# Optimization experiments

Measured on AMD Instinct MI355X. Metric: run time of the kernel, lower is better.

The kernel has to match this reference:

```python
import jax, jax.numpy as jnp
import numpy as np

RATIO = 4

def positional_encoding(d_model, max_len, w_s):
    # w_s: (B,) per-example frequency warp. pe[b, p, 0::2]=sin, pe[b, p, 1::2]=cos
    pos = jnp.arange(max_len, dtype=jnp.float32)                      # (L,)
    div = jnp.power(10000.0, jnp.arange(0, d_model, 2, dtype=jnp.float32) / d_model)  # (d/2,)
    ang = w_s[:, None, None] * pos[None, :, None] / div[None, None, :]  # (B, L, d/2)
    pe = jnp.stack([jnp.sin(ang), jnp.cos(ang)], axis=-1)             # (B, L, d/2, 2)
    return pe.reshape(w_s.shape[0], max_len, d_model)

def setup_inputs() -> dict:
    key = jax.random.key(0)
    ks = jax.random.split(key, 6)
    B, Tds, L, D = 32, 2048, 512, 256
    q = jax.random.normal(ks[0], (B, Tds, D), dtype=jnp.float32)
    k = jax.random.normal(ks[1], (B, L, D), dtype=jnp.float32)
    v = jax.random.normal(ks[2], (B, L, D), dtype=jnp.float32)
    w_compress = jax.random.normal(ks[3], (D // RATIO, D), dtype=jnp.float32) * (D ** -0.5)
    text_lengths = jax.random.randint(ks[4], (B,), L // 2, L + 1).at[0].set(L)
    mel_lengths = jax.random.randint(ks[5], (B,), (Tds * RATIO) // 2, Tds * RATIO + 1).at[0].set(Tds * RATIO)
    return {"q": q, "k": k, "v": v, "w_compress": w_compress,
            "text_lengths": text_lengths, "mel_lengths": mel_lengths}

def reference(q, k, v, w_compress, text_lengths, mel_lengths):
    B, Tds, D = q.shape
    L = k.shape[1]
    # padding masks (True = padded)
    text_mask = jnp.arange(L)[None, :] >= text_lengths[:, None]            # (B, L)
    mel_mask_ds = jnp.arange(Tds)[None, :] >= (mel_lengths // RATIO)[:, None]  # (B, Tds)
    # positional encodings
    q = q + positional_encoding(D, Tds, jnp.ones((B,), dtype=jnp.float32))
    w_s = mel_lengths.astype(jnp.float32) / RATIO / text_lengths.astype(jnp.float32)
    k = k + positional_encoding(D, L, w_s)
    q = q * (float(D) ** -0.5)
    # scores + masked softmax over text axis
    scores = jnp.einsum('btd,bld->btl', q, k)                              # (B, Tds, L)
    scores = jnp.where(text_mask[:, None, :], -jnp.inf, scores)
    align = jax.nn.softmax(scores, axis=-1)
    align = jnp.where(mel_mask_ds[:, :, None], 0.0, align)
    # hard argmax one-hot, straight-through blend
    idx = jnp.argmax(align, axis=-1)                                       # (B, Tds)
    align_oh = jax.nn.one_hot(idx, L, dtype=align.dtype)
    align_oh = jnp.where(mel_mask_ds[:, :, None], 0.0, align_oh)
    blend = align + jax.lax.stop_gradient(align_oh - align)
    attn = jnp.einsum('btl,bld->btd', blend, v)                            # (B, Tds, D)
    # Compress (Linear D -> D//ratio, no bias) then transpose(1,2)
    out = jnp.einsum('btd,cd->bct', attn, w_compress)                      # (B, D//ratio, Tds)
    return out, align
```

## Files before the change

### kernel.cpp

```cpp
#include <hip/hip_runtime.h>
#include <math.h>

#define NB  32
#define TDS 2048
#define LL  512
#define DD  256
#define DC  64
#define GAP_THR 4e-4f

typedef __attribute__((ext_vector_type(8)))  short short8;
typedef __attribute__((ext_vector_type(16))) float f32x16;
typedef __attribute__((ext_vector_type(4)))  float f32x4;

__device__ __forceinline__ unsigned short f2bf(float x) {
    union { float f; unsigned u; } v; v.f = x;
    unsigned r = v.u + 0x7fffu + ((v.u >> 16) & 1u);
    return (unsigned short)(r >> 16);
}
__device__ __forceinline__ float bf2f(unsigned short h) {
    union { unsigned u; float f; } v; v.u = ((unsigned)h) << 16;
    return v.f;
}


__global__ void peq_kernel(float* __restrict__ peq, int* __restrict__ cnt) {
    int idx = blockIdx.x * 256 + threadIdx.x;
    if (idx == 0) cnt[0] = 0;
    int t = idx >> 8;
    int d = idx & 255;
    int i = d >> 1;
    double invdiv = exp((double)i * (-9.210340371976184 / 128.0));
    double ang = (double)t * invdiv;
    double s, c;
    sincos(ang, &s, &c);
    peq[idx] = (float)((d & 1) ? c : s);
}

__global__ __launch_bounds__(256)
void pek_kernel(const float* __restrict__ k,
                const int* __restrict__ text_lengths,
                const int* __restrict__ mel_lengths,
                char* __restrict__ kps) {
    __shared__ double invdiv[128];
    const int tid = threadIdx.x;
    if (tid < 128) invdiv[tid] = exp((double)tid * (-9.210340371976184 / 128.0));
    __syncthreads();
    int f = blockIdx.x * 256 + tid;
    int b = f >> 14;
    int r = f & 16383;
    int ks = r >> 11;
    int r2 = r & 2047;
    int cs = r2 >> 7;
    int r3 = r2 & 127;
    int kh = r3 >> 6;
    int g  = (r3 >> 5) & 1;
    int lane32 = r3 & 31;
    int l  = cs * 32 + lane32;
    int k0 = ks * 32 + kh * 16 + g * 8;
    const float* kr = k + ((size_t)(b * LL + l)) * DD + k0;
    float4 kv0 = *(const float4*)(kr);
    float4 kv1 = *(const float4*)(kr + 4);
    float kv[8] = {kv0.x, kv0.y, kv0.z, kv0.w, kv1.x, kv1.y, kv1.z, kv1.w};
    double wsd = ((double)mel_lengths[b] * 0.25) / (double)text_lengths[b];
    double base_ang = wsd * (double)l;
    unsigned short h[8], lo8[8];
#pragma unroll
    for (int jj = 0; jj < 4; ++jj) {
        int i = (k0 >> 1) + jj;
        double ang = base_ang * invdiv[i];
        double n = rint(ang * 0.15915494309189535);
        double red = fma(n, -6.283185307179586, ang);
        float sn, cs2;
        sincosf((float)red, &sn, &cs2);
        float e0 = kv[2 * jj] + sn;
        float e1 = kv[2 * jj + 1] + cs2;
        h[2 * jj]       = f2bf(e0);
        h[2 * jj + 1]   = f2bf(e1);
        lo8[2 * jj]     = f2bf(e0 - bf2f(h[2 * jj]));
        lo8[2 * jj + 1] = f2bf(e1 - bf2f(h[2 * jj + 1]));
    }
    size_t off = (size_t)b * 524288 + (size_t)ks * 65536 + (size_t)cs * 4096
               + kh * 1024 + g * 512 + lane32 * 16;
    uint4 hv, lv;
    hv.x = h[0] | ((unsigned)h[1] << 16); hv.y = h[2] | ((unsigned)h[3] << 16);
    hv.z = h[4] | ((unsigned)h[5] << 16); hv.w = h[6] | ((unsigned)h[7] << 16);
    lv.x = lo8[0] | ((unsigned)lo8[1] << 16); lv.y = lo8[2] | ((unsigned)lo8[3] << 16);
    lv.z = lo8[4] | ((unsigned)lo8[5] << 16); lv.w = lo8[6] | ((unsigned)lo8[7] << 16);
    *(uint4*)(kps + off) = hv;
    *(uint4*)(kps + off + 2048) = lv;
}

__global__ __launch_bounds__(256, 4)
void score_kernel(const float* __restrict__ q,
                  const float* __restrict__ peq,
                  const char* __restrict__ kps,
                  const int* __restrict__ text_lengths,
                  const int* __restrict__ mel_lengths,
                  float* __restrict__ align_out,
                  int* __restrict__ idx_out,
                  int* __restrict__ flag_cnt,
                  int* __restrict__ flags) {
    __shared__ alignas(16) char smA[32768];
    struct Epi {
        float v1[4][32]; int i1[4][32]; float v2[4][32];
        float S[4][32];  float M[32];
    };
    __shared__ Epi ep;

    const int wgid = blockIdx.x;
    const int xcd = wgid & 7, loc = wgid >> 3;
    const int nid = xcd * 256 + loc;
    const int b  = nid >> 6;
    const int t0 = (nid & 63) << 5;

    const int tid = threadIdx.x;
    const int wn = tid >> 6, lane = tid & 63;
    const int c31 = lane & 31, hi5 = lane >> 5;
    const int tlen = text_lengths[b];
    const int melq = mel_lengths[b] >> 2;

    const char* kpb = kps + (size_t)b * 524288 + (size_t)(hi5 * 512 + c31 * 16);

    f32x16 acc[4];
#pragma unroll
    for (int ci = 0; ci < 4; ++ci)
#pragma unroll
        for (int rg = 0; rg < 16; ++rg) acc[ci][rg] = 0.f;

#define BLOAD(dst, ksv, civ)                                                    \
    {                                                                           \
        const char* p = kpb + (ksv) * 65536 + (wn * 4 + (civ)) * 4096;          \
        dst[0] = *(const short8*)(p);                                           \
        dst[1] = *(const short8*)(p + 1024);                                    \
        dst[2] = *(const short8*)(p + 2048);                                    \
        dst[3] = *(const short8*)(p + 3072);                                    \
    }
#define MFMA6(CI, B)                                                            \
    {                                                                           \
        acc[CI] = __builtin_amdgcn_mfma_f32_32x32x16_bf16(ah0, B[0], acc[CI], 0, 0, 0); \
        acc[CI] = __builtin_amdgcn_mfma_f32_32x32x16_bf16(ah0, B[2], acc[CI], 0, 0, 0); \
        acc[CI] = __builtin_amdgcn_mfma_f32_32x32x16_bf16(al0, B[0], acc[CI], 0, 0, 0); \
        acc[CI] = __builtin_amdgcn_mfma_f32_32x32x16_bf16(ah1, B[1], acc[CI], 0, 0, 0); \
        acc[CI] = __builtin_amdgcn_mfma_f32_32x32x16_bf16(ah1, B[3], acc[CI], 0, 0, 0); \
        acc[CI] = __builtin_amdgcn_mfma_f32_32x32x16_bf16(al1, B[1], acc[CI], 0, 0, 0); \
    }

    short8 B0[4], B1[4];
    BLOAD(B0, 0, 0)

    {
        const int sr = tid >> 3, kc = tid & 7;
        const float* qr = q   + ((size_t)(b * TDS) + t0 + sr) * DD;
        const float* pr = peq + (size_t)(t0 + sr) * DD;
#pragma unroll
        for (int kq = 0; kq < 4; ++kq) {
            int m = kq * 8 + kc;
            int k0 = m * 8;
            float4 qa = *(const float4*)(qr + k0);
            float4 qb4 = *(const float4*)(qr + k0 + 4);
            float4 pa = *(const float4*)(pr + k0);
            float4 pb = *(const float4*)(pr + k0 + 4);
            float e[8] = {(qa.x + pa.x) * 0.0625f, (qa.y + pa.y) * 0.0625f,
                          (qa.z + pa.z) * 0.0625f, (qa.w + pa.w) * 0.0625f,
                          (qb4.x + pb.x) * 0.0625f, (qb4.y + pb.y) * 0.0625f,
                          (qb4.z + pb.z) * 0.0625f, (qb4.w + pb.w) * 0.0625f};
            unsigned short h[8], lo[8];
#pragma unroll
            for (int j = 0; j < 8; ++j) {
                h[j] = f2bf(e[j]);
                lo[j] = f2bf(e[j] - bf2f(h[j]));
            }
            uint4 hv, lv;
            hv.x = h[0] | ((unsigned)h[1] << 16); hv.y = h[2] | ((unsigned)h[3] << 16);
            hv.z = h[4] | ((unsigned)h[5] << 16); hv.w = h[6] | ((unsigned)h[7] << 16);
            lv.x = lo[0] | ((unsigned)lo[1] << 16); lv.y = lo[2] | ((unsigned)lo[3] << 16);
            lv.z = lo[4] | ((unsigned)lo[5] << 16); lv.w = lo[6] | ((unsigned)lo[7] << 16);
            int base = (m >> 2) * 4096 + ((m >> 1) & 1) * 1024 + (m & 1) * 512 + sr * 16;
            *(uint4*)(smA + base) = hv;
            *(uint4*)(smA + base + 2048) = lv;
        }
    }
    __syncthreads();

    const int afr = hi5 * 512 + c31 * 16;
    for (int ks = 0; ks < 8; ++ks) {
        const char* ab = smA + ks * 4096 + afr;
        short8 ah0 = *(const short8*)(ab);
        short8 ah1 = *(const short8*)(ab + 1024);
        short8 al0 = *(const short8*)(ab + 2048);
        short8 al1 = *(const short8*)(ab + 3072);
        BLOAD(B1, ks, 1)
        MFMA6(0, B0)
        BLOAD(B0, ks, 2)
        MFMA6(1, B1)
        BLOAD(B1, ks, 3)
        MFMA6(2, B0)
        if (ks < 7) BLOAD(B0, ks + 1, 0)
        MFMA6(3, B1)
    }
#undef BLOAD
#undef MFMA6

    const float NEGINF = -__builtin_inff();
#pragma unroll
    for (int ci = 0; ci < 4; ++ci) {
        int col = wn * 128 + ci * 32 + c31;
        if (col >= tlen) {
#pragma unroll
            for (int rg = 0; rg < 16; ++rg) acc[ci][rg] = NEGINF;
        }
    }
    float v1[16]; int i1[16]; float v2[16];
#pragma unroll
    for (int rg = 0; rg < 16; ++rg) {
        v1[rg] = acc[0][rg]; i1[rg] = wn * 128 + c31; v2[rg] = NEGINF;
#pragma unroll
        for (int ci = 1; ci < 4; ++ci) {
            float v = acc[ci][rg]; int col = wn * 128 + ci * 32 + c31;
            if (v > v1[rg]) { v2[rg] = v1[rg]; v1[rg] = v; i1[rg] = col; }
            else if (v > v2[rg]) v2[rg] = v;
        }
    }
#pragma unroll
    for (int off = 1; off <= 16; off <<= 1) {
#pragma unroll
        for (int rg = 0; rg < 16; ++rg) {
            float ov1 = __shfl_xor(v1[rg], off, 64);
            int   oi1 = __shfl_xor(i1[rg], off, 64);
            float ov2 = __shfl_xor(v2[rg], off, 64);
            if (ov1 > v1[rg]) { v2[rg] = fmaxf(v1[rg], ov2); v1[rg] = ov1; i1[rg] = oi1; }
            else if (ov1 < v1[rg]) { v2[rg] = fmaxf(v2[rg], ov1); }
            else { i1[rg] = min(i1[rg], oi1); v2[rg] = v1[rg]; }
        }
    }
    if (c31 == 0) {
#pragma unroll
        for (int rg = 0; rg < 16; ++rg) {
            int r32 = (rg & 3) + 8 * (rg >> 2) + 4 * hi5;
            ep.v1[wn][r32] = v1[rg]; ep.i1[wn][r32] = i1[rg]; ep.v2[wn][r32] = v2[rg];
        }
    }
    __syncthreads();
    {
        const int r32 = c31;
        float V1 = ep.v1[0][r32]; int I1 = ep.i1[0][r32]; float V2 = ep.v2[0][r32];
#pragma unroll
        for (int w = 1; w < 4; ++w) {
            float cv1 = ep.v1[w][r32]; int ci1 = ep.i1[w][r32]; float cv2 = ep.v2[w][r32];
            if (cv1 > V1) { V2 = fmaxf(V1, cv2); V1 = cv1; I1 = ci1; }
            else if (cv1 < V1) { V2 = fmaxf(V2, cv1); }
            else { V2 = V1; }
        }
        if (wn == 0 && hi5 == 0) {
            int t = t0 + r32;
            idx_out[b * TDS + t] = I1;
            if (t < melq && (V1 - V2) < GAP_THR) {
                int pos = atomicAdd(flag_cnt, 1);
                flags[pos] = (b << 11) | t;
            }
            ep.M[r32] = V1;
        }
    }
    __syncthreads();
    float ssum[16];
#pragma unroll
    for (int rg = 0; rg < 16; ++rg) {
        int r32 = (rg & 3) + 8 * (rg >> 2) + 4 * hi5;
        float M = ep.M[r32];
        float s = 0.f;
#pragma unroll
        for (int ci = 0; ci < 4; ++ci) {
            float p = __expf(acc[ci][rg] - M);
            acc[ci][rg] = p; s += p;
        }
        ssum[rg] = s;
    }
#pragma unroll
    for (int off = 1; off <= 16; off <<= 1)
#pragma unroll
        for (int rg = 0; rg < 16; ++rg) ssum[rg] += __shfl_xor(ssum[rg], off, 64);
    if (c31 == 0) {
#pragma unroll
        for (int rg = 0; rg < 16; ++rg) {
            int r32 = (rg & 3) + 8 * (rg >> 2) + 4 * hi5;
            ep.S[wn][r32] = ssum[rg];
        }
    }
    __syncthreads();
#pragma unroll
    for (int rg = 0; rg < 16; ++rg) {
        int r32 = (rg & 3) + 8 * (rg >> 2) + 4 * hi5;
        int t = t0 + r32;
        float denom = ep.S[0][r32] + ep.S[1][r32] + ep.S[2][r32] + ep.S[3][r32];
        float sc = (t < melq) ? (1.0f / denom) : 0.f;
        size_t obase = ((size_t)(b * TDS + t)) * LL + wn * 128 + c31;
#pragma unroll
        for (int ci = 0; ci < 4; ++ci)
            __builtin_nontemporal_store(acc[ci][rg] * sc, align_out + obase + ci * 32);
    }
}

__global__ __launch_bounds__(256)
void refine_kernel(const float* __restrict__ q,
                   const float* __restrict__ k,
                   const int* __restrict__ text_lengths,
                   const int* __restrict__ mel_lengths,
                   const int* __restrict__ flags,
                   const int* __restrict__ flag_cnt,
                   int* __restrict__ idx_out) {
    __shared__ double qd[DD];
    __shared__ double invdiv[128];
    __shared__ double rbest[4];
    __shared__ int    ribest[4];
    const int tid = threadIdx.x;
    if (tid < 128)
        invdiv[tid] = 1.0 / pow(10000.0, (double)tid * (1.0 / 128.0));
    const int cnt = flag_cnt[0];
    for (int r = blockIdx.x; r < cnt; r += gridDim.x) {
        const int code = flags[r];
        const int b = code >> 11, t = code & 2047;
        const int tlen = text_lengths[b];
        const double ws = ((double)mel_lengths[b] * 0.25) / (double)text_lengths[b];
        __syncthreads();
        {
            const int d = tid, i = d >> 1;
            double ang = (double)t * invdiv[i];
            double sn, cs;
            sincos(ang, &sn, &cs);
            qd[d] = ((double)q[((size_t)b * TDS + t) * DD + d] + ((d & 1) ? cs : sn)) * 0.0625;
        }
        __syncthreads();
        double best = -1.0e300; int bi = 0x7fffffff;
        for (int p = 0; p < 2; ++p) {
            const int l = tid + p * 256;
            if (l < tlen) {
                const float* kr = k + ((size_t)b * LL + l) * DD;
                const double wl = ws * (double)l;
                double sacc = 0.0;
                for (int i = 0; i < 128; ++i) {
                    double ang = wl * invdiv[i];
                    double sn, cs;
                    sincos(ang, &sn, &cs);
                    sacc += ((double)kr[2 * i]     + sn) * qd[2 * i];
                    sacc += ((double)kr[2 * i + 1] + cs) * qd[2 * i + 1];
                }
                if (sacc > best || (sacc == best && l < bi)) { best = sacc; bi = l; }
            }
        }
        for (int off = 1; off <= 32; off <<= 1) {
            double ov = __shfl_xor(best, off, 64);
            int   oi = __shfl_xor(bi, off, 64);
            if (ov > best || (ov == best && oi < bi)) { best = ov; bi = oi; }
        }
        const int wv = tid >> 6;
        if ((tid & 63) == 0) { rbest[wv] = best; ribest[wv] = bi; }
        __syncthreads();
        if (tid == 0) {
            double bb = rbest[0]; int ii = ribest[0];
            for (int w = 1; w < 4; ++w)
                if (rbest[w] > bb || (rbest[w] == bb && ribest[w] < ii)) { bb = rbest[w]; ii = ribest[w]; }
            idx_out[b * TDS + t] = ii;
        }
    }
}

__global__ __launch_bounds__(256, 4)
void compress_kernel(const float* __restrict__ v,
                     const float* __restrict__ wc,
                     const int* __restrict__ idx_in,
                     const int* __restrict__ mel_lengths,
                     float* __restrict__ out) {
    __shared__ float Ws[256 * 68];
    __shared__ float Vs[16 * 132];
    __shared__ int   idxs[128];
    const int b   = blockIdx.y;
    const int t0  = blockIdx.x * 128;
    const int tid = threadIdx.x;
    const int melq = mel_lengths[b] >> 2;
    const float* vb = v + (size_t)b * LL * DD;

    if (tid < 128) {
        int t = t0 + tid;
        int ii = idx_in[b * TDS + t];
        idxs[tid] = (t >= melq) ? -1 : ii;
    }
#pragma unroll
    for (int r = 0; r < 16; ++r) {
        int f = tid + r * 256;
        int c = f >> 6;
        int u = f & 63;
        float4 wv = *(const float4*)(wc + (size_t)c * DD + u * 4);
        Ws[(u * 4 + 0) * 68 + c] = wv.x;
        Ws[(u * 4 + 1) * 68 + c] = wv.y;
        Ws[(u * 4 + 2) * 68 + c] = wv.z;
        Ws[(u * 4 + 3) * 68 + c] = wv.w;
    }

    const int tx = tid & 7;
    const int ty = tid >> 3;
    const int tv = tid >> 2;
    const int uv = tid & 3;
    float acc[8][4];
#pragma unroll
    for (int i = 0; i < 8; ++i)
#pragma unroll
        for (int j = 0; j < 4; ++j) acc[i][j] = 0.f;

    for (int ks = 0; ks < 16; ++ks) {
        const int d0 = ks * 16;
        __syncthreads();
#pragma unroll
        for (int p = 0; p < 2; ++p) {
            int t = tv + p * 64;
            int row = idxs[t];
            float4 vv = make_float4(0.f, 0.f, 0.f, 0.f);
            if (row >= 0) vv = *(const float4*)(vb + (size_t)row * DD + d0 + uv * 4);
            Vs[(uv * 4 + 0) * 132 + t] = vv.x;
            Vs[(uv * 4 + 1) * 132 + t] = vv.y;
            Vs[(uv * 4 + 2) * 132 + t] = vv.z;
            Vs[(uv * 4 + 3) * 132 + t] = vv.w;
        }
        __syncthreads();
#pragma unroll
        for (int kk = 0; kk < 16; ++kk) {
            const float* wrow = Ws + (size_t)(d0 + kk) * 68 + tx * 8;
            float4 a0 = *(const float4*)(wrow);
            float4 a1 = *(const float4*)(wrow + 4);
            float4 bb = *(const float4*)(Vs + kk * 132 + ty * 4);
            const float av[8] = {a0.x, a0.y, a0.z, a0.w, a1.x, a1.y, a1.z, a1.w};
            const float bv[4] = {bb.x, bb.y, bb.z, bb.w};
#pragma unroll
            for (int i = 0; i < 8; ++i)
#pragma unroll
                for (int j = 0; j < 4; ++j)
                    acc[i][j] = fmaf(av[i], bv[j], acc[i][j]);
        }
    }
#pragma unroll
    for (int ci = 0; ci < 8; ++ci) {
        int c = tx * 8 + ci;
        f32x4 o = {acc[ci][0], acc[ci][1], acc[ci][2], acc[ci][3]};
        __builtin_nontemporal_store(o, (f32x4*)(out + ((size_t)(b * DC + c)) * TDS + t0 + ty * 4));
    }
}

extern "C" void kernel_launch(void* const* d_in, const int* in_sizes, int n_in,
                              void* d_out, int out_size, void* d_ws, size_t ws_size,
                              hipStream_t stream) {
    const float* q    = (const float*)d_in[0];
    const float* k    = (const float*)d_in[1];
    const float* v    = (const float*)d_in[2];
    const float* wc   = (const float*)d_in[3];
    const int*   text = (const int*)d_in[4];
    const int*   mel  = (const int*)d_in[5];

    float* out   = (float*)d_out;
    float* align = out + (size_t)NB * DC * TDS;

    char*  wsb = (char*)d_ws;
    char*  KPS = wsb;
    float* PEQ = (float*)(wsb + 16777216);
    int*   IDX = (int*)(wsb + 16777216 + 2097152);
    int*   CNT = IDX + (size_t)NB * TDS;
    int*   FLG = CNT + 1;

    hipLaunchKernelGGL(peq_kernel, dim3(TDS * DD / 256), dim3(256), 0, stream, PEQ, CNT);
    hipLaunchKernelGGL(pek_kernel, dim3(NB * 16384 / 256), dim3(256), 0, stream,
                       k, text, mel, KPS);
    hipLaunchKernelGGL(score_kernel, dim3(2048), dim3(256), 0, stream,
                       q, PEQ, KPS, text, mel, align, IDX, CNT, FLG);
    hipLaunchKernelGGL(refine_kernel, dim3(256), dim3(256), 0, stream,
                       q, k, text, mel, FLG, CNT, IDX);
    hipLaunchKernelGGL(compress_kernel, dim3(TDS / 128, NB), dim3(256), 0, stream,
                       v, wc, IDX, mel, out);
}
```

Before: 223.4 us.

## Double score tile rows per block and shrink compress tiles with streamed weights

The score kernel now uses 512-thread blocks covering 64 query rows, with two row-groups of four waves each. Each group shares the same K fragments, so K traffic from global/L2 is halved, at the cost of doubling A-tile LDS to 64KB and lowering occupancy. The compress kernel drops its full 64KB transposed weight staging in favour of streaming 16-wide weight slices per k-step, uses 64-column tiles with a 2-column-per-thread micro-tile, and replaces nontemporal float4 stores with plain float2 stores. This cuts LDS use and raises block count, but adds more global weight reloads and lowers register-level reuse.

```diff
diff --git a/kernel.cpp b/kernel.cpp
--- a/kernel.cpp
+++ b/kernel.cpp
@@ -10,7 +10,6 @@
 
 typedef __attribute__((ext_vector_type(8)))  short short8;
 typedef __attribute__((ext_vector_type(16))) float f32x16;
-typedef __attribute__((ext_vector_type(4)))  float f32x4;
 
 __device__ __forceinline__ unsigned short f2bf(float x) {
     union { float f; unsigned u; } v; v.f = x;
@@ -90,7 +89,7 @@
     *(uint4*)(kps + off + 2048) = lv;
 }
 
-__global__ __launch_bounds__(256, 4)
+__global__ __launch_bounds__(512, 2)
 void score_kernel(const float* __restrict__ q,
                   const float* __restrict__ peq,
                   const char* __restrict__ kps,
@@ -100,21 +99,22 @@
                   int* __restrict__ idx_out,
                   int* __restrict__ flag_cnt,
                   int* __restrict__ flags) {
-    __shared__ alignas(16) char smA[32768];
+    __shared__ alignas(16) char smA[65536];
     struct Epi {
-        float v1[4][32]; int i1[4][32]; float v2[4][32];
-        float S[4][32];  float M[32];
+        float v1[2][4][32]; int i1[2][4][32]; float v2[2][4][32];
+        float S[2][4][32];  float M[2][32];
     };
     __shared__ Epi ep;
 
     const int wgid = blockIdx.x;
     const int xcd = wgid & 7, loc = wgid >> 3;
-    const int nid = xcd * 256 + loc;
-    const int b  = nid >> 6;
-    const int t0 = (nid & 63) << 5;
+    const int nid = xcd * 128 + loc;
+    const int b  = nid >> 5;
+    const int t0 = (nid & 31) << 6;
 
     const int tid = threadIdx.x;
-    const int wn = tid >> 6, lane = tid & 63;
+    const int wid = tid >> 6, lane = tid & 63;
+    const int wm = wid >> 2, wn = wid & 3;
     const int c31 = lane & 31, hi5 = lane >> 5;
     const int tlen = text_lengths[b];
     const int melq = mel_lengths[b] >> 2;
@@ -175,16 +175,17 @@
             hv.z = h[4] | ((unsigned)h[5] << 16); hv.w = h[6] | ((unsigned)h[7] << 16);
             lv.x = lo[0] | ((unsigned)lo[1] << 16); lv.y = lo[2] | ((unsigned)lo[3] << 16);
             lv.z = lo[4] | ((unsigned)lo[5] << 16); lv.w = lo[6] | ((unsigned)lo[7] << 16);
-            int base = (m >> 2) * 4096 + ((m >> 1) & 1) * 1024 + (m & 1) * 512 + sr * 16;
+            int base = (m >> 2) * 8192 + (sr >> 5) * 4096 + ((m >> 1) & 1) * 1024
+                     + (m & 1) * 512 + (sr & 31) * 16;
             *(uint4*)(smA + base) = hv;
             *(uint4*)(smA + base + 2048) = lv;
         }
     }
     __syncthreads();
 
-    const int afr = hi5 * 512 + c31 * 16;
+    const int afr = wm * 4096 + hi5 * 512 + c31 * 16;
     for (int ks = 0; ks < 8; ++ks) {
-        const char* ab = smA + ks * 4096 + afr;
+        const char* ab = smA + ks * 8192 + afr;
         short8 ah0 = *(const short8*)(ab);
         short8 ah1 = *(const short8*)(ab + 1024);
         short8 al0 = *(const short8*)(ab + 2048);
@@ -237,28 +238,28 @@
 #pragma unroll
         for (int rg = 0; rg < 16; ++rg) {
             int r32 = (rg & 3) + 8 * (rg >> 2) + 4 * hi5;
-            ep.v1[wn][r32] = v1[rg]; ep.i1[wn][r32] = i1[rg]; ep.v2[wn][r32] = v2[rg];
+            ep.v1[wm][wn][r32] = v1[rg]; ep.i1[wm][wn][r32] = i1[rg]; ep.v2[wm][wn][r32] = v2[rg];
         }
     }
     __syncthreads();
     {
         const int r32 = c31;
-        float V1 = ep.v1[0][r32]; int I1 = ep.i1[0][r32]; float V2 = ep.v2[0][r32];
+        float V1 = ep.v1[wm][0][r32]; int I1 = ep.i1[wm][0][r32]; float V2 = ep.v2[wm][0][r32];
 #pragma unroll
         for (int w = 1; w < 4; ++w) {
-            float cv1 = ep.v1[w][r32]; int ci1 = ep.i1[w][r32]; float cv2 = ep.v2[w][r32];
+            float cv1 = ep.v1[wm][w][r32]; int ci1 = ep.i1[wm][w][r32]; float cv2 = ep.v2[wm][w][r32];
             if (cv1 > V1) { V2 = fmaxf(V1, cv2); V1 = cv1; I1 = ci1; }
             else if (cv1 < V1) { V2 = fmaxf(V2, cv1); }
             else { V2 = V1; }
         }
         if (wn == 0 && hi5 == 0) {
-            int t = t0 + r32;
+            int t = t0 + wm * 32 + r32;
             idx_out[b * TDS + t] = I1;
             if (t < melq && (V1 - V2) < GAP_THR) {
                 int pos = atomicAdd(flag_cnt, 1);
                 flags[pos] = (b << 11) | t;
             }
-            ep.M[r32] = V1;
+            ep.M[wm][r32] = V1;
         }
     }
     __syncthreads();
@@ -266,7 +267,7 @@
 #pragma unroll
     for (int rg = 0; rg < 16; ++rg) {
         int r32 = (rg & 3) + 8 * (rg >> 2) + 4 * hi5;
-        float M = ep.M[r32];
+        float M = ep.M[wm][r32];
         float s = 0.f;
 #pragma unroll
         for (int ci = 0; ci < 4; ++ci) {
@@ -283,15 +284,15 @@
 #pragma unroll
         for (int rg = 0; rg < 16; ++rg) {
             int r32 = (rg & 3) + 8 * (rg >> 2) + 4 * hi5;
-            ep.S[wn][r32] = ssum[rg];
+            ep.S[wm][wn][r32] = ssum[rg];
         }
     }
     __syncthreads();
 #pragma unroll
     for (int rg = 0; rg < 16; ++rg) {
         int r32 = (rg & 3) + 8 * (rg >> 2) + 4 * hi5;
-        int t = t0 + r32;
-        float denom = ep.S[0][r32] + ep.S[1][r32] + ep.S[2][r32] + ep.S[3][r32];
+        int t = t0 + wm * 32 + r32;
+        float denom = ep.S[wm][0][r32] + ep.S[wm][1][r32] + ep.S[wm][2][r32] + ep.S[wm][3][r32];
         float sc = (t < melq) ? (1.0f / denom) : 0.f;
         size_t obase = ((size_t)(b * TDS + t)) * LL + wn * 128 + c31;
 #pragma unroll
@@ -364,83 +365,72 @@
     }
 }
 
-__global__ __launch_bounds__(256, 4)
+__global__ __launch_bounds__(256)
 void compress_kernel(const float* __restrict__ v,
                      const float* __restrict__ wc,
                      const int* __restrict__ idx_in,
                      const int* __restrict__ mel_lengths,
                      float* __restrict__ out) {
-    __shared__ float Ws[256 * 68];
-    __shared__ float Vs[16 * 132];
-    __shared__ int   idxs[128];
+    __shared__ float Ws[16 * 68];
+    __shared__ float Vs[16 * 68];
+    __shared__ int   idxs[64];
     const int b   = blockIdx.y;
-    const int t0  = blockIdx.x * 128;
+    const int t0  = blockIdx.x * 64;
     const int tid = threadIdx.x;
     const int melq = mel_lengths[b] >> 2;
     const float* vb = v + (size_t)b * LL * DD;
 
-    if (tid < 128) {
+    if (tid < 64) {
         int t = t0 + tid;
         int ii = idx_in[b * TDS + t];
         idxs[tid] = (t >= melq) ? -1 : ii;
     }
-#pragma unroll
-    for (int r = 0; r < 16; ++r) {
-        int f = tid + r * 256;
-        int c = f >> 6;
-        int u = f & 63;
-        float4 wv = *(const float4*)(wc + (size_t)c * DD + u * 4);
-        Ws[(u * 4 + 0) * 68 + c] = wv.x;
-        Ws[(u * 4 + 1) * 68 + c] = wv.y;
-        Ws[(u * 4 + 2) * 68 + c] = wv.z;
-        Ws[(u * 4 + 3) * 68 + c] = wv.w;
-    }
-
-    const int tx = tid & 7;
-    const int ty = tid >> 3;
-    const int tv = tid >> 2;
-    const int uv = tid & 3;
-    float acc[8][4];
-#pragma unroll
-    for (int i = 0; i < 8; ++i)
-#pragma unroll
-        for (int j = 0; j < 4; ++j) acc[i][j] = 0.f;
+
+    const int tx = tid >> 5;
+    const int ty = tid & 31;
+    const int sc = tid >> 2;
+    const int su = tid & 3;
+    float acc[8][2];
+#pragma unroll
+    for (int i = 0; i < 8; ++i) { acc[i][0] = 0.f; acc[i][1] = 0.f; }
 
     for (int ks = 0; ks < 16; ++ks) {
         const int d0 = ks * 16;
         __syncthreads();
-#pragma unroll
-        for (int p = 0; p < 2; ++p) {
-            int t = tv + p * 64;
-            int row = idxs[t];
+        {
+            float4 wv = *(const float4*)(wc + (size_t)sc * DD + d0 + su * 4);
+            Ws[(su * 4 + 0) * 68 + sc] = wv.x;
+            Ws[(su * 4 + 1) * 68 + sc] = wv.y;
+            Ws[(su * 4 + 2) * 68 + sc] = wv.z;
+            Ws[(su * 4 + 3) * 68 + sc] = wv.w;
+            int row = idxs[sc];
             float4 vv = make_float4(0.f, 0.f, 0.f, 0.f);
-            if (row >= 0) vv = *(const float4*)(vb + (size_t)row * DD + d0 + uv * 4);
-            Vs[(uv * 4 + 0) * 132 + t] = vv.x;
-            Vs[(uv * 4 + 1) * 132 + t] = vv.y;
-            Vs[(uv * 4 + 2) * 132 + t] = vv.z;
-            Vs[(uv * 4 + 3) * 132 + t] = vv.w;
+            if (row >= 0) vv = *(const float4*)(vb + (size_t)row * DD + d0 + su * 4);
+            Vs[(su * 4 + 0) * 68 + sc] = vv.x;
+            Vs[(su * 4 + 1) * 68 + sc] = vv.y;
+            Vs[(su * 4 + 2) * 68 + sc] = vv.z;
+            Vs[(su * 4 + 3) * 68 + sc] = vv.w;
         }
         __syncthreads();
 #pragma unroll
         for (int kk = 0; kk < 16; ++kk) {
-            const float* wrow = Ws + (size_t)(d0 + kk) * 68 + tx * 8;
+            const float* wrow = Ws + kk * 68 + tx * 8;
             float4 a0 = *(const float4*)(wrow);
             float4 a1 = *(const float4*)(wrow + 4);
-            float4 bb = *(const float4*)(Vs + kk * 132 + ty * 4);
+            float2 bb = *(const float2*)(Vs + kk * 68 + ty * 2);
             const float av[8] = {a0.x, a0.y, a0.z, a0.w, a1.x, a1.y, a1.z, a1.w};
-            const float bv[4] = {bb.x, bb.y, bb.z, bb.w};
-#pragma unroll
-            for (int i = 0; i < 8; ++i)
-#pragma unroll
-                for (int j = 0; j < 4; ++j)
-                    acc[i][j] = fmaf(av[i], bv[j], acc[i][j]);
-        }
-    }
-#pragma unroll
-    for (int ci = 0; ci < 8; ++ci) {
-        int c = tx * 8 + ci;
-        f32x4 o = {acc[ci][0], acc[ci][1], acc[ci][2], acc[ci][3]};
-        __builtin_nontemporal_store(o, (f32x4*)(out + ((size_t)(b * DC + c)) * TDS + t0 + ty * 4));
+#pragma unroll
+            for (int i = 0; i < 8; ++i) {
+                acc[i][0] = fmaf(av[i], bb.x, acc[i][0]);
+                acc[i][1] = fmaf(av[i], bb.y, acc[i][1]);
+            }
+        }
+    }
+#pragma unroll
+    for (int i = 0; i < 8; ++i) {
+        int c = tx * 8 + i;
+        float2 o = make_float2(acc[i][0], acc[i][1]);
+        *(float2*)(out + ((size_t)(b * DC + c)) * TDS + t0 + ty * 2) = o;
     }
 }
 
@@ -467,10 +457,10 @@
     hipLaunchKernelGGL(peq_kernel, dim3(TDS * DD / 256), dim3(256), 0, stream, PEQ, CNT);
     hipLaunchKernelGGL(pek_kernel, dim3(NB * 16384 / 256), dim3(256), 0, stream,
                        k, text, mel, KPS);
-    hipLaunchKernelGGL(score_kernel, dim3(2048), dim3(256), 0, stream,
+    hipLaunchKernelGGL(score_kernel, dim3(1024), dim3(512), 0, stream,
                        q, PEQ, KPS, text, mel, align, IDX, CNT, FLG);
     hipLaunchKernelGGL(refine_kernel, dim3(256), dim3(256), 0, stream,
                        q, k, text, mel, FLG, CNT, IDX);
-    hipLaunchKernelGGL(compress_kernel, dim3(TDS / 128, NB), dim3(256), 0, stream,
+    hipLaunchKernelGGL(compress_kernel, dim3(TDS / 64, NB), dim3(256), 0, stream,
                        v, wc, IDX, mel, out);
 }
```

New measurement: 882.6 us. +295.1%, slower.
